# Performance work log

Measured on AMD Instinct MI355X. Metric: run time of the kernel, lower is better.

Reference implementation:

```python
import jax, jax.numpy as jnp
import numpy as np

D_MODEL = 512
N_HEADS = 8
D_K = 64
N_GENE = 16384
N_TF = 512


def setup_inputs() -> dict:
    key = jax.random.key(0)
    ks = jax.random.split(key, 12)
    HD = N_HEADS * D_K
    s = 1.0 / np.sqrt(D_MODEL)
    inp = {
        "H_TF": jax.random.normal(ks[0], (N_TF, D_MODEL), jnp.float32),
        "H_G": jax.random.normal(ks[1], (N_GENE, D_MODEL), jnp.float32),
        "z_exp": jax.random.normal(ks[2], (N_GENE, D_MODEL), jnp.float32),
        "z_seq": jax.random.normal(ks[3], (N_GENE, D_MODEL), jnp.float32),
        "z_txt": jax.random.normal(ks[4], (N_GENE, D_MODEL), jnp.float32),
        "tf_idx": jax.random.randint(ks[5], (N_TF,), 0, N_GENE, jnp.int64)
        if jax.config.jax_enable_x64 else jax.random.randint(ks[5], (N_TF,), 0, N_GENE, jnp.int32),
        "Wq_seq": jax.random.normal(ks[6], (D_MODEL, HD), jnp.float32) * s,
        "Wk_seq": jax.random.normal(ks[7], (D_MODEL, HD), jnp.float32) * s,
        "Wq_exp": jax.random.normal(ks[8], (D_MODEL, HD), jnp.float32) * s,
        "Wk_exp": jax.random.normal(ks[9], (D_MODEL, HD), jnp.float32) * s,
        "Wq_txt": jax.random.normal(ks[10], (D_MODEL, HD), jnp.float32) * s,
        "Wk_txt": jax.random.normal(ks[11], (D_MODEL, HD), jnp.float32) * s,
        # gate initialized as identity per head, zero bias (as in nn.init.eye_)
        "gate_weight": jnp.tile(jnp.eye(3, dtype=jnp.float32)[None], (N_HEADS, 1, 1)),
        "gate_bias": jnp.zeros((N_HEADS, 3), jnp.float32),
    }
    return inp


def reference(H_TF, H_G, z_exp, z_seq, z_txt, tf_idx,
              Wq_seq, Wk_seq, Wq_exp, Wk_exp, Wq_txt, Wk_txt,
              gate_weight, gate_bias):
    n_tf, n_gene = H_TF.shape[0], H_G.shape[0]
    H, dk = N_HEADS, D_K
    scale = jnp.sqrt(jnp.asarray(dk, H_TF.dtype))

    def qk_score(z, Wq, Wk):
        Q = (z[tf_idx] @ Wq).reshape(n_tf, H, dk)   # [t,h,d]
        K = (z @ Wk).reshape(n_gene, H, dk)          # [g,h,d]
        return jnp.einsum('thd,ghd->htg', Q, K) / scale  # [h,t,g]

    s_bind = qk_score(z_seq, Wq_seq, Wk_seq)
    s_coexpr = qk_score(z_exp, Wq_exp, Wk_exp)
    s_know = qk_score(z_txt, Wq_txt, Wk_txt)

    # evidence gate: per-head 3x3 mixing + softmax over evidence axis
    s = jnp.stack([s_bind, s_coexpr, s_know], axis=-1)        # [h,t,g,3]
    gate_logits = jnp.einsum('htge,hef->htgf', s, gate_weight) + gate_bias[:, None, None, :]
    alpha = jax.nn.softmax(gate_logits, axis=-1)               # [h,t,g,3]

    u = alpha[..., 0] * s_bind + alpha[..., 1] * s_coexpr + alpha[..., 2] * s_know
    A = jax.nn.softmax(u, axis=-1)                             # softmax over genes

    u_mean = u.mean(axis=0)          # [t,g]
    A_mean = A.mean(axis=0)          # [t,g]
    alpha_mean = alpha.mean(axis=0)  # [t,g,3]
    return (H_TF, H_G, A_mean, u_mean, alpha_mean)
```

## Files before the change

kernel.cpp:

```cpp
#include <hip/hip_runtime.h>
#include <hip/hip_bf16.h>
#include <stdint.h>

typedef __attribute__((ext_vector_type(4))) float f32x4;
typedef __attribute__((ext_vector_type(8))) short bf16x8;
typedef __attribute__((ext_vector_type(8))) unsigned short u16x8;

#define N_GENE 16384
#define N_TF   512
#define DMODEL 512
#define L2E    1.44269504088896340736f

__device__ __forceinline__ float bf2f(unsigned short u) {
    union { unsigned int i; float f; } v; v.i = ((unsigned int)u) << 16; return v.f;
}
__device__ __forceinline__ unsigned short f2bf(float f) {
    unsigned int r;
    asm("v_cvt_pk_bf16_f32 %0, %1, %1" : "=v"(r) : "v"(f));
    return (unsigned short)r;
}
__device__ __forceinline__ float fast_rcp(float x) {
    float r; asm("v_rcp_f32 %0, %1" : "=v"(r) : "v"(x)); return r;
}
__device__ __forceinline__ float fast_exp2(float x) {
    float r; asm("v_exp_f32 %0, %1" : "=v"(r) : "v"(x)); return r;
}

#define GLOBAL_AS(p) ((const __attribute__((address_space(1))) void*)(p))
#define LDS_AS(p)    ((__attribute__((address_space(3))) void*)(p))

__global__ __launch_bounds__(256) void prep(const float* __restrict__ z0, const float* __restrict__ z1,
                                            const float* __restrict__ z2, unsigned short* __restrict__ zb,
                                            const float* __restrict__ w0, const float* __restrict__ w1,
                                            const float* __restrict__ w2, const float* __restrict__ w3,
                                            const float* __restrict__ w4, const float* __restrict__ w5,
                                            unsigned short* __restrict__ wt, float* __restrict__ lp) {
    __shared__ unsigned short tile[32][33];
    const int b = blockIdx.x;
    const int tid = threadIdx.x;
    if (b < 12288) {
        const float* s = b < 4096 ? z0 : (b < 8192 ? z1 : z2);
        const int m = b >> 12;
        const int blk = b & 4095;
        size_t i = ((size_t)blk * 256 + tid) * 8;
        float4 a = *(const float4*)(s + i);
        float4 c = *(const float4*)(s + i + 4);
        unsigned int q0, q1, q2, q3;
        asm("v_cvt_pk_bf16_f32 %0, %1, %2" : "=v"(q0) : "v"(a.x), "v"(a.y));
        asm("v_cvt_pk_bf16_f32 %0, %1, %2" : "=v"(q1) : "v"(a.z), "v"(a.w));
        asm("v_cvt_pk_bf16_f32 %0, %1, %2" : "=v"(q2) : "v"(c.x), "v"(c.y));
        asm("v_cvt_pk_bf16_f32 %0, %1, %2" : "=v"(q3) : "v"(c.z), "v"(c.w));
        uint4 o; o.x = q0; o.y = q1; o.z = q2; o.w = q3;
        *(uint4*)(zb + (size_t)m * (size_t)N_GENE * 512 + i) = o;
    } else if (b < 13824) {
        const float* srcs[6] = { w0, w1, w2, w3, w4, w5 };
        const int b2 = b - 12288;
        const int m = b2 >> 8;
        const int rem = b2 & 255;
        const int by = rem >> 4, bx = rem & 15;
        const int tx = tid & 31, ty8 = tid >> 5;
        const float* src = srcs[m];
        const int x = bx * 32 + tx;
        const int y0 = by * 32;
        for (int i = ty8; i < 32; i += 8)
            tile[i][tx] = f2bf(src[(size_t)(y0 + i) * 512 + x]);
        __syncthreads();
        const int xo = by * 32 + tx;
        const int yo0 = bx * 32;
        unsigned short* d = wt + (size_t)m * 512 * 512;
        for (int i = ty8; i < 32; i += 8)
            d[(size_t)(yo0 + i) * 512 + xo] = tile[tx][i];
    } else {
        for (int i = tid; i < 8 * N_TF; i += 256) lp[i] = 0.f;
    }
}

__global__ __launch_bounds__(256) void gemm_all(const unsigned short* __restrict__ Zb,
                                                const unsigned short* __restrict__ Wt,
                                                unsigned short* __restrict__ Kp,
                                                unsigned short* __restrict__ Qp,
                                                const int* __restrict__ tf_idx) {
    __shared__ unsigned short As[128 * 64];
    __shared__ unsigned short Bs[128 * 64];
    const int e = blockIdx.z;
    const unsigned short* A = Zb + (size_t)e * N_GENE * 512;
    const unsigned short* Bt;
    unsigned short* C;
    const int* idx;
    int mBase;
    if (blockIdx.y < 128) {
        Bt = Wt + (size_t)(e * 2 + 1) * 262144;
        C = Kp + (size_t)e * N_GENE * 512;
        idx = nullptr;
        mBase = blockIdx.y * 128;
    } else {
        Bt = Wt + (size_t)(e * 2) * 262144;
        C = Qp + (size_t)e * 512 * 512;
        idx = tf_idx;
        mBase = (blockIdx.y - 128) * 128;
    }
    const int tid = threadIdx.x;
    const int lane = tid & 63;
    const int w = tid >> 6;
    const int nBase = blockIdx.x * 128;
    const int wm = (w & 1) * 64;
    const int wn = (w >> 1) * 64;
    const int lm = lane & 15, lq = lane >> 4;

    const int rbase = tid >> 3;
    const int seg = tid & 7;
    const int scol = ((seg ^ (rbase & 7)) << 3);
    const unsigned short* aSrc[4];
    const unsigned short* bSrc[4];
    #pragma unroll
    for (int i = 0; i < 4; ++i) {
        int r = i * 32 + rbase;
        int ar = idx ? idx[mBase + r] : (mBase + r);
        aSrc[i] = A + (size_t)ar * 512 + scol;
        bSrc[i] = Bt + (size_t)(nBase + r) * 512 + scol;
    }
    const int ldsOfs = (tid & 192) * 8;

    f32x4 acc[4][4] = {};

    for (int k0 = 0; k0 < 512; k0 += 64) {
        #pragma unroll
        for (int i = 0; i < 4; ++i) {
            __builtin_amdgcn_global_load_lds(GLOBAL_AS(aSrc[i] + k0), LDS_AS(As + i * 2048 + ldsOfs), 16, 0, 0);
            __builtin_amdgcn_global_load_lds(GLOBAL_AS(bSrc[i] + k0), LDS_AS(Bs + i * 2048 + ldsOfs), 16, 0, 0);
        }
        __syncthreads();
        bf16x8 af[4][2], bfr[4][2];
        #pragma unroll
        for (int mt = 0; mt < 4; ++mt) {
            int row = wm + mt * 16 + lm;
            int sw = row & 7;
            #pragma unroll
            for (int hh = 0; hh < 2; ++hh)
                af[mt][hh] = *(const bf16x8*)(As + row * 64 + (((hh * 4 + lq) ^ sw) << 3));
        }
        #pragma unroll
        for (int nt = 0; nt < 4; ++nt) {
            int row = wn + nt * 16 + lm;
            int sw = row & 7;
            #pragma unroll
            for (int hh = 0; hh < 2; ++hh)
                bfr[nt][hh] = *(const bf16x8*)(Bs + row * 64 + (((hh * 4 + lq) ^ sw) << 3));
        }
        #pragma unroll
        for (int mt = 0; mt < 4; ++mt)
            #pragma unroll
            for (int nt = 0; nt < 4; ++nt) {
                acc[mt][nt] = __builtin_amdgcn_mfma_f32_16x16x32_bf16(af[mt][0], bfr[nt][0], acc[mt][nt], 0, 0, 0);
                acc[mt][nt] = __builtin_amdgcn_mfma_f32_16x16x32_bf16(af[mt][1], bfr[nt][1], acc[mt][nt], 0, 0, 0);
            }
        __syncthreads();
    }
    #pragma unroll
    for (int mt = 0; mt < 4; ++mt)
        #pragma unroll
        for (int nt = 0; nt < 4; ++nt)
            #pragma unroll
            for (int r = 0; r < 4; ++r) {
                int m = mBase + wm + mt * 16 + lq * 4 + r;
                int n = nBase + wn + nt * 16 + lm;
                C[(size_t)m * 512 + n] = f2bf(acc[mt][nt][r]);
            }
}

__global__ __launch_bounds__(256, 4) void score_pass(const unsigned short* __restrict__ Qp,
                                                     const unsigned short* __restrict__ Kp,
                                                     const float* __restrict__ gw,
                                                     const float* __restrict__ gb,
                                                     unsigned short* __restrict__ p_out,
                                                     float* __restrict__ l_out,
                                                     float* __restrict__ u_mean,
                                                     float* __restrict__ alpha_mean)
{
    __shared__ unsigned short pbuf[4][32 * 40];
    const int tid = threadIdx.x;
    const int lane = tid & 63;
    const int w = tid >> 6;
    const int bid = blockIdx.x;
    const int o = (bid & 7) * 256 + (bid >> 3);
    const int gx = o >> 3;
    const int ty = o & 7;
    const int tw = ty * 64 + (w & 1) * 32;
    const int g0 = gx * 64 + (w >> 1) * 32;
    const int lm = lane & 15, lq = lane >> 4;
    unsigned short* pw = &pbuf[w][0];

    float u_sum[2][2][4] = {};
    float a0_sum[2][2][4] = {};
    float a1_sum[2][2][4] = {};

    #pragma unroll 1
    for (int h = 0; h < 8; ++h) {
        float W2[3][3], B2[3];
        #pragma unroll
        for (int e = 0; e < 3; ++e)
            #pragma unroll
            for (int f = 0; f < 3; ++f) W2[e][f] = gw[(h * 3 + e) * 3 + f] * (0.125f * L2E);
        #pragma unroll
        for (int f = 0; f < 3; ++f) B2[f] = gb[h * 3 + f] * L2E;

        f32x4 s[3][2][2];
        #pragma unroll
        for (int e = 0; e < 3; ++e) {
            const unsigned short* qbase = Qp + (size_t)e * 512 * 512 + (size_t)(tw + lm) * 512 + h * 64 + lq * 8;
            const unsigned short* kbase = Kp + (size_t)e * N_GENE * 512 + (size_t)(g0 + lm) * 512 + h * 64 + lq * 8;
            bf16x8 q[2][2], k[2][2];
            #pragma unroll
            for (int mt = 0; mt < 2; ++mt) {
                q[mt][0] = *(const bf16x8*)(qbase + mt * 16 * 512);
                q[mt][1] = *(const bf16x8*)(qbase + mt * 16 * 512 + 32);
            }
            #pragma unroll
            for (int nt = 0; nt < 2; ++nt) {
                k[nt][0] = *(const bf16x8*)(kbase + nt * 16 * 512);
                k[nt][1] = *(const bf16x8*)(kbase + nt * 16 * 512 + 32);
            }
            #pragma unroll
            for (int mt = 0; mt < 2; ++mt)
                #pragma unroll
                for (int nt = 0; nt < 2; ++nt) {
                    f32x4 a = {};
                    a = __builtin_amdgcn_mfma_f32_16x16x32_bf16(q[mt][0], k[nt][0], a, 0, 0, 0);
                    a = __builtin_amdgcn_mfma_f32_16x16x32_bf16(q[mt][1], k[nt][1], a, 0, 0, 0);
                    s[e][mt][nt] = a;
                }
        }
        float lpart[2][4] = {};
        #pragma unroll
        for (int mt = 0; mt < 2; ++mt)
            #pragma unroll
            for (int nt = 0; nt < 2; ++nt) {
                #pragma unroll
                for (int r = 0; r < 4; ++r) {
                    float s0 = s[0][mt][nt][r];
                    float s1 = s[1][mt][nt][r];
                    float s2 = s[2][mt][nt][r];
                    float gl0 = fmaf(s2, W2[2][0], fmaf(s1, W2[1][0], fmaf(s0, W2[0][0], B2[0])));
                    float gl1 = fmaf(s2, W2[2][1], fmaf(s1, W2[1][1], fmaf(s0, W2[0][1], B2[1])));
                    float gl2 = fmaf(s2, W2[2][2], fmaf(s1, W2[1][2], fmaf(s0, W2[0][2], B2[2])));
                    float e0 = fast_exp2(gl0), e1 = fast_exp2(gl1), e2 = fast_exp2(gl2);
                    float rz = fast_rcp(e0 + e1 + e2);
                    float a0 = e0 * rz, a1 = e1 * rz;
                    float dot = fmaf(e0, s0, fmaf(e1, s1, e2 * s2));
                    float u = dot * (rz * 0.125f);
                    float pv = fast_exp2(u * L2E);
                    u_sum[mt][nt][r] += u;
                    a0_sum[mt][nt][r] += a0;
                    a1_sum[mt][nt][r] += a1;
                    lpart[mt][r] += pv;
                    pw[(mt * 16 + lq * 4 + r) * 40 + nt * 16 + lm] = f2bf(pv);
                }
            }
        {
            const int rrow = lane >> 1, half = lane & 1;
            const unsigned short* src = pw + rrow * 40 + half * 16;
            bf16x8 v0 = *(const bf16x8*)(src);
            bf16x8 v1 = *(const bf16x8*)(src + 8);
            unsigned short* pg = p_out + ((size_t)h * N_TF + (tw + rrow)) * (size_t)N_GENE + (g0 + half * 16);
            __builtin_nontemporal_store(v0, (bf16x8*)pg);
            __builtin_nontemporal_store(v1, (bf16x8*)(pg + 8));
        }
        #pragma unroll
        for (int mt = 0; mt < 2; ++mt)
            #pragma unroll
            for (int r = 0; r < 4; ++r) {
                float v = lpart[mt][r];
                v += __shfl_xor(v, 1);
                v += __shfl_xor(v, 2);
                v += __shfl_xor(v, 4);
                v += __shfl_xor(v, 8);
                if (lm == 0) atomicAdd(&l_out[h * N_TF + tw + mt * 16 + lq * 4 + r], v);
            }
    }
    #pragma unroll
    for (int mt = 0; mt < 2; ++mt)
        #pragma unroll
        for (int nt = 0; nt < 2; ++nt)
            #pragma unroll
            for (int r = 0; r < 4; ++r) {
                int t = tw + mt * 16 + lq * 4 + r;
                int g = g0 + nt * 16 + lm;
                __builtin_nontemporal_store(u_sum[mt][nt][r] * 0.125f, u_mean + (size_t)t * N_GENE + g);
                float a0m = a0_sum[mt][nt][r] * 0.125f;
                float a1m = a1_sum[mt][nt][r] * 0.125f;
                size_t base = ((size_t)t * N_GENE + g) * 3;
                alpha_mean[base + 0] = a0m;
                alpha_mean[base + 1] = a1m;
                alpha_mean[base + 2] = 1.0f - a0m - a1m;
            }
}

__global__ __launch_bounds__(256) void finalize_A(const unsigned short* __restrict__ p,
                                                  const float* __restrict__ l,
                                                  float* __restrict__ A_mean) {
    const int t = blockIdx.x;
    float rinv[8];
    #pragma unroll
    for (int h = 0; h < 8; ++h) rinv[h] = 0.125f / l[h * N_TF + t];
    const int gbase = blockIdx.y * 4096 + threadIdx.x * 8;
    #pragma unroll
    for (int gg = 0; gg < 2; ++gg) {
        int g8 = gbase + gg * 2048;
        float s[8] = {};
        #pragma unroll
        for (int h = 0; h < 8; ++h) {
            u16x8 pv = __builtin_nontemporal_load((const u16x8*)(p + ((size_t)h * N_TF + t) * N_GENE + g8));
            float r = rinv[h];
            #pragma unroll
            for (int j = 0; j < 8; ++j) s[j] += bf2f(pv[j]) * r;
        }
        f32x4 o0, o1;
        o0[0] = s[0]; o0[1] = s[1]; o0[2] = s[2]; o0[3] = s[3];
        o1[0] = s[4]; o1[1] = s[5]; o1[2] = s[6]; o1[3] = s[7];
        __builtin_nontemporal_store(o0, (f32x4*)(A_mean + (size_t)t * N_GENE + g8));
        __builtin_nontemporal_store(o1, (f32x4*)(A_mean + (size_t)t * N_GENE + g8 + 4));
    }
}

__global__ __launch_bounds__(256) void copy_all(const int4* __restrict__ a, const int4* __restrict__ b,
                                                int4* __restrict__ da, int4* __restrict__ db) {
    const int bx = blockIdx.x;
    if (bx < 256) {
        int i = bx * 256 + threadIdx.x;
        da[i] = a[i];
    } else {
        int i = (bx - 256) * 256 + threadIdx.x;
        db[i] = b[i];
    }
}

extern "C" void kernel_launch(void* const* d_in, const int* in_sizes, int n_in,
                              void* d_out, int out_size, void* d_ws, size_t ws_size,
                              hipStream_t stream) {
    const float* H_TF  = (const float*)d_in[0];
    const float* H_G   = (const float*)d_in[1];
    const float* z[3]  = { (const float*)d_in[3], (const float*)d_in[2], (const float*)d_in[4] };
    const int* tf_idx  = (const int*)d_in[5];
    const float* Wq[3] = { (const float*)d_in[6], (const float*)d_in[8], (const float*)d_in[10] };
    const float* Wk[3] = { (const float*)d_in[7], (const float*)d_in[9], (const float*)d_in[11] };
    const float* gw    = (const float*)d_in[12];
    const float* gb    = (const float*)d_in[13];
    float* out = (float*)d_out;

    float* out_HTF   = out;
    float* out_HG    = out + 262144;
    float* out_Amean = out + 262144 + 8388608;
    float* out_umean = out + 262144 + 8388608 + 8388608;
    float* out_alpha = out + 262144 + 8388608 + 8388608 + 8388608;

    unsigned short* Wt = (unsigned short*)d_ws;
    unsigned short* Kp = Wt + 6 * 262144;
    unsigned short* Qp = Kp + 3 * (size_t)N_GENE * 512;
    unsigned short* Pp = Qp + 3 * 512 * 512;
    float*          Lp = (float*)(Pp + (size_t)8 * N_TF * N_GENE);
    unsigned short* Zb = Pp;

    prep<<<13825, 256, 0, stream>>>(z[0], z[1], z[2], Zb,
                                    Wq[0], Wk[0], Wq[1], Wk[1], Wq[2], Wk[2], Wt, Lp);

    gemm_all<<<dim3(4, 132, 3), 256, 0, stream>>>(Zb, Wt, Kp, Qp, tf_idx);

    score_pass<<<2048, 256, 0, stream>>>(Qp, Kp, gw, gb, Pp, Lp, out_umean, out_alpha);

    finalize_A<<<dim3(512, 4), 256, 0, stream>>>(Pp, Lp, out_Amean);

    copy_all<<<256 + 8192, 256, 0, stream>>>((const int4*)H_TF, (const int4*)H_G,
                                             (int4*)out_HTF, (int4*)out_HG);
}
```

Before: 692.4 us.

## Prefetch next-head K fragments and stage alpha_mean stores through LDS

Reorganizes score_pass. K fragments for the next head are loaded into registers while the current head's gate math runs, Q fragments are loaded directly per evidence type, and the output tile of alpha_mean is staged in shared memory so it can be written as contiguous 16-byte nontemporal vector stores instead of strided scalar stores. The min-blocks launch bound is dropped, and shared memory grows to 25.6 KB per block. The extra live K registers may lower occupancy.

New measurement: 641.7 us. 1.08x faster.

```diff
diff --git a/kernel.cpp b/kernel.cpp
--- a/kernel.cpp
+++ b/kernel.cpp
@@ -168,16 +168,16 @@
             }
 }
 
-__global__ __launch_bounds__(256, 4) void score_pass(const unsigned short* __restrict__ Qp,
-                                                     const unsigned short* __restrict__ Kp,
-                                                     const float* __restrict__ gw,
-                                                     const float* __restrict__ gb,
-                                                     unsigned short* __restrict__ p_out,
-                                                     float* __restrict__ l_out,
-                                                     float* __restrict__ u_mean,
-                                                     float* __restrict__ alpha_mean)
+__global__ __launch_bounds__(256) void score_pass(const unsigned short* __restrict__ Qp,
+                                                  const unsigned short* __restrict__ Kp,
+                                                  const float* __restrict__ gw,
+                                                  const float* __restrict__ gb,
+                                                  unsigned short* __restrict__ p_out,
+                                                  float* __restrict__ l_out,
+                                                  float* __restrict__ u_mean,
+                                                  float* __restrict__ alpha_mean)
 {
-    __shared__ unsigned short pbuf[4][32 * 40];
+    __shared__ float abuf[4][1600];
     const int tid = threadIdx.x;
     const int lane = tid & 63;
     const int w = tid >> 6;
@@ -188,12 +188,26 @@
     const int tw = ty * 64 + (w & 1) * 32;
     const int g0 = gx * 64 + (w >> 1) * 32;
     const int lm = lane & 15, lq = lane >> 4;
-    unsigned short* pw = &pbuf[w][0];
+    unsigned short* pw = (unsigned short*)(&abuf[w][0]);
 
     float u_sum[2][2][4] = {};
     float a0_sum[2][2][4] = {};
     float a1_sum[2][2][4] = {};
 
+    const unsigned short* qbase0 = Qp + (size_t)(tw + lm) * 512 + lq * 8;
+    const unsigned short* kbase0 = Kp + (size_t)(g0 + lm) * 512 + lq * 8;
+
+    bf16x8 kf[3][2][2];
+    #pragma unroll
+    for (int e = 0; e < 3; ++e) {
+        const unsigned short* kb_ = kbase0 + (size_t)e * N_GENE * 512;
+        #pragma unroll
+        for (int nt = 0; nt < 2; ++nt) {
+            kf[e][nt][0] = *(const bf16x8*)(kb_ + nt * 16 * 512);
+            kf[e][nt][1] = *(const bf16x8*)(kb_ + nt * 16 * 512 + 32);
+        }
+    }
+
     #pragma unroll 1
     for (int h = 0; h < 8; ++h) {
         float W2[3][3], B2[3];
@@ -207,34 +221,41 @@
         f32x4 s[3][2][2];
         #pragma unroll
         for (int e = 0; e < 3; ++e) {
-            const unsigned short* qbase = Qp + (size_t)e * 512 * 512 + (size_t)(tw + lm) * 512 + h * 64 + lq * 8;
-            const unsigned short* kbase = Kp + (size_t)e * N_GENE * 512 + (size_t)(g0 + lm) * 512 + h * 64 + lq * 8;
-            bf16x8 q[2][2], k[2][2];
-            #pragma unroll
-            for (int mt = 0; mt < 2; ++mt) {
-                q[mt][0] = *(const bf16x8*)(qbase + mt * 16 * 512);
-                q[mt][1] = *(const bf16x8*)(qbase + mt * 16 * 512 + 32);
-            }
+            const unsigned short* qb_ = qbase0 + (size_t)e * 512 * 512 + h * 64;
+            bf16x8 q00 = *(const bf16x8*)(qb_);
+            bf16x8 q01 = *(const bf16x8*)(qb_ + 32);
+            bf16x8 q10 = *(const bf16x8*)(qb_ + 16 * 512);
+            bf16x8 q11 = *(const bf16x8*)(qb_ + 16 * 512 + 32);
             #pragma unroll
             for (int nt = 0; nt < 2; ++nt) {
-                k[nt][0] = *(const bf16x8*)(kbase + nt * 16 * 512);
-                k[nt][1] = *(const bf16x8*)(kbase + nt * 16 * 512 + 32);
-            }
-            #pragma unroll
-            for (int mt = 0; mt < 2; ++mt)
+                f32x4 a = {};
+                a = __builtin_amdgcn_mfma_f32_16x16x32_bf16(q00, kf[e][nt][0], a, 0, 0, 0);
+                a = __builtin_amdgcn_mfma_f32_16x16x32_bf16(q01, kf[e][nt][1], a, 0, 0, 0);
+                s[e][0][nt] = a;
+                f32x4 b = {};
+                b = __builtin_amdgcn_mfma_f32_16x16x32_bf16(q10, kf[e][nt][0], b, 0, 0, 0);
+                b = __builtin_amdgcn_mfma_f32_16x16x32_bf16(q11, kf[e][nt][1], b, 0, 0, 0);
+                s[e][1][nt] = b;
+            }
+        }
+
+        if (h < 7) {
+            #pragma unroll
+            for (int e = 0; e < 3; ++e) {
+                const unsigned short* kb_ = kbase0 + (size_t)e * N_GENE * 512 + (h + 1) * 64;
                 #pragma unroll
                 for (int nt = 0; nt < 2; ++nt) {
-                    f32x4 a = {};
-                    a = __builtin_amdgcn_mfma_f32_16x16x32_bf16(q[mt][0], k[nt][0], a, 0, 0, 0);
-                    a = __builtin_amdgcn_mfma_f32_16x16x32_bf16(q[mt][1], k[nt][1], a, 0, 0, 0);
-                    s[e][mt][nt] = a;
+                    kf[e][nt][0] = *(const bf16x8*)(kb_ + nt * 16 * 512);
+                    kf[e][nt][1] = *(const bf16x8*)(kb_ + nt * 16 * 512 + 32);
                 }
-        }
+            }
+        }
+
         float lpart[2][4] = {};
         #pragma unroll
         for (int mt = 0; mt < 2; ++mt)
             #pragma unroll
-            for (int nt = 0; nt < 2; ++nt) {
+            for (int nt = 0; nt < 2; ++nt)
                 #pragma unroll
                 for (int r = 0; r < 4; ++r) {
                     float s0 = s[0][mt][nt][r];
@@ -255,7 +276,6 @@
                     lpart[mt][r] += pv;
                     pw[(mt * 16 + lq * 4 + r) * 40 + nt * 16 + lm] = f2bf(pv);
                 }
-            }
         {
             const int rrow = lane >> 1, half = lane & 1;
             const unsigned short* src = pw + rrow * 40 + half * 16;
@@ -277,22 +297,37 @@
                 if (lm == 0) atomicAdd(&l_out[h * N_TF + tw + mt * 16 + lq * 4 + r], v);
             }
     }
-    #pragma unroll
-    for (int mt = 0; mt < 2; ++mt)
+
+    #pragma unroll
+    for (int mt = 0; mt < 2; ++mt) {
         #pragma unroll
         for (int nt = 0; nt < 2; ++nt)
             #pragma unroll
             for (int r = 0; r < 4; ++r) {
-                int t = tw + mt * 16 + lq * 4 + r;
-                int g = g0 + nt * 16 + lm;
-                __builtin_nontemporal_store(u_sum[mt][nt][r] * 0.125f, u_mean + (size_t)t * N_GENE + g);
+                const int row = lq * 4 + r;
+                const int colg = nt * 16 + lm;
+                __builtin_nontemporal_store(u_sum[mt][nt][r] * 0.125f,
+                                            u_mean + (size_t)(tw + mt * 16 + row) * N_GENE + g0 + colg);
                 float a0m = a0_sum[mt][nt][r] * 0.125f;
                 float a1m = a1_sum[mt][nt][r] * 0.125f;
-                size_t base = ((size_t)t * N_GENE + g) * 3;
-                alpha_mean[base + 0] = a0m;
-                alpha_mean[base + 1] = a1m;
-                alpha_mean[base + 2] = 1.0f - a0m - a1m;
-            }
+                float* ab = &abuf[w][row * 100 + colg * 3];
+                ab[0] = a0m;
+                ab[1] = a1m;
+                ab[2] = 1.0f - a0m - a1m;
+            }
+        {
+            const int drow = lane & 15;
+            const int dk = lane >> 4;
+            const float* srcb = &abuf[w][drow * 100];
+            float* dst = alpha_mean + (size_t)(tw + mt * 16 + drow) * (N_GENE * 3) + (size_t)g0 * 3;
+            #pragma unroll
+            for (int j = 0; j < 6; ++j) {
+                const int c = (j * 4 + dk) * 4;
+                f32x4 v = *(const f32x4*)(srcb + c);
+                __builtin_nontemporal_store(v, (f32x4*)(dst + c));
+            }
+        }
+    }
 }
 
 __global__ __launch_bounds__(256) void finalize_A(const unsigned short* __restrict__ p,
```
